# Kernel tuning notes

Measured on AMD Instinct MI355X. Metric: run time of the kernel, lower is better.

## Reference

```python
import jax, jax.numpy as jnp
import numpy as np

N = 10000   # nodes
E = 100000  # edges (before self-loops)
H = 4       # heads (layers 0-3); last layer uses 1 head
C = 200     # out_channels per head
IN_DIMS = [200, H * C, H * C, H * C, H * C]
HEADS   = [H, H, H, H, 1]
NEG_SLOPE = 0.2  # PyG GATConv default


def _gat_layer(x, src, dst, W, a_src, a_dst, b, heads):
    # x: [N, Fin], W: [Fin, heads*C], a_src/a_dst: [heads, C], b: [heads*C]
    h = (x @ W).reshape(N, heads, C)                       # [N,H,C]
    alpha_src = jnp.einsum('nhc,hc->nh', h, a_src)         # [N,H]
    alpha_dst = jnp.einsum('nhc,hc->nh', h, a_dst)         # [N,H]
    e = jax.nn.leaky_relu(alpha_src[src] + alpha_dst[dst], NEG_SLOPE)  # [E',H]
    # segment softmax over incoming edges of each dst node
    m = jax.ops.segment_max(e, dst, num_segments=N)        # [N,H]
    ex = jnp.exp(e - m[dst])                               # [E',H]
    den = jax.ops.segment_sum(ex, dst, num_segments=N)     # [N,H]
    alpha = ex / den[dst]                                  # [E',H]
    out = jax.ops.segment_sum(h[src] * alpha[:, :, None], dst, num_segments=N)
    return out.reshape(N, heads * C) + b, alpha


def setup_inputs() -> dict:
    key = jax.random.key(0)
    ks = jax.random.split(key, 2 + 4 * 5)
    inp = {}
    inp['X'] = jax.random.normal(ks[0], (N, 200), jnp.float32)
    inp['edge_index'] = jax.random.randint(ks[1], (2, E), 0, N, dtype=jnp.int32)
    k = 2
    for i in range(5):
        fin, hd = IN_DIMS[i], HEADS[i]
        s = 1.0 / np.sqrt(fin)
        inp[f'W{i}'] = jax.random.normal(ks[k], (fin, hd * C), jnp.float32) * s; k += 1
        inp[f'as{i}'] = jax.random.normal(ks[k], (hd, C), jnp.float32) * s; k += 1
        inp[f'ad{i}'] = jax.random.normal(ks[k], (hd, C), jnp.float32) * s; k += 1
        inp[f'b{i}'] = jnp.zeros((hd * C,), jnp.float32); k += 1
    return inp


def reference(X, edge_index,
              W0, as0, ad0, b0, W1, as1, ad1, b1, W2, as2, ad2, b2,
              W3, as3, ad3, b3, W4, as4, ad4, b4):
    # add self-loops (PyG GATConv default add_self_loops=True)
    loops = jnp.arange(N, dtype=edge_index.dtype)
    src = jnp.concatenate([edge_index[0], loops])
    dst = jnp.concatenate([edge_index[1], loops])
    gelu = lambda v: jax.nn.gelu(v, approximate=False)
    # eval mode: all dropouts are identity
    x, _ = _gat_layer(X, src, dst, W0, as0, ad0, b0, HEADS[0]); x = gelu(x)
    x, _ = _gat_layer(x, src, dst, W1, as1, ad1, b1, HEADS[1]); x = gelu(x)
    x, _ = _gat_layer(x, src, dst, W2, as2, ad2, b2, HEADS[2]); x = gelu(x)
    x, _ = _gat_layer(x, src, dst, W3, as3, ad3, b3, HEADS[3]); x = gelu(x)
    x, edge_attn = _gat_layer(x, src, dst, W4, as4, ad4, b4, HEADS[4])
    x = gelu(x)
    return (x, edge_attn)
```

## Files before the change

### kernel.cpp

```cpp
#include <hip/hip_runtime.h>
#include <math.h>

#define NN 10000
#define EE 100000
#define EPE 110000
#define CC 200
#define MPAD 10112

typedef __attribute__((ext_vector_type(8))) _Float16 f16x8;
typedef __attribute__((ext_vector_type(4))) _Float16 f16x4;
typedef __attribute__((ext_vector_type(4))) unsigned short u16x4;
typedef __attribute__((ext_vector_type(4))) float f32x4;

__device__ __forceinline__ float lrelu(float v) { return v >= 0.f ? v : 0.2f * v; }
__device__ __forceinline__ float gelu_f(float v) { return 0.5f * v * (1.f + erff(v * 0.70710678118654752f)); }


__global__ void build_edges_kernel(const int* __restrict__ ei,
                                   int* __restrict__ src_all, int* __restrict__ dst_all,
                                   int* __restrict__ deg) {
    int e = blockIdx.x * blockDim.x + threadIdx.x;
    if (e >= EPE) return;
    int s, d;
    if (e < EE) { s = ei[e]; d = ei[EE + e]; }
    else        { s = e - EE; d = e - EE; }
    src_all[e] = s;
    dst_all[e] = d;
    atomicAdd(&deg[d], 1);
}

__global__ void scan_kernel(const int* __restrict__ deg, int* __restrict__ row_ptr, int n) {
    __shared__ int wsum[16];
    int tid = threadIdx.x;
    int lane = tid & 63, w = tid >> 6;
    int carry = 0;
    for (int base = 0; base < n; base += 1024) {
        int idx = base + tid;
        int v = (idx < n) ? deg[idx] : 0;
        int x = v;
#pragma unroll
        for (int off = 1; off < 64; off <<= 1) {
            int t = __shfl_up(x, off);
            if (lane >= off) x += t;
        }
        if (lane == 63) wsum[w] = x;
        __syncthreads();
        if (w == 0) {
            int s = (lane < 16) ? wsum[lane] : 0;
#pragma unroll
            for (int off = 1; off < 16; off <<= 1) {
                int t = __shfl_up(s, off);
                if (lane >= off) s += t;
            }
            if (lane < 16) wsum[lane] = s;
        }
        __syncthreads();
        int woff = (w > 0) ? wsum[w - 1] : 0;
        if (idx < n) row_ptr[idx] = carry + woff + x - v;
        carry += wsum[15];
        __syncthreads();
    }
    if (tid == 0) row_ptr[n] = carry;
}

__global__ void scatter_kernel(const int* __restrict__ src_all, const int* __restrict__ dst_all,
                               const int* __restrict__ row_ptr, int* __restrict__ cursor,
                               int* __restrict__ col_src, int* __restrict__ col_eid) {
    int e = blockIdx.x * blockDim.x + threadIdx.x;
    if (e >= EPE) return;
    int d = dst_all[e];
    int pos = row_ptr[d] + atomicAdd(&cursor[d], 1);
    col_src[pos] = src_all[e];
    col_eid[pos] = e;
}


__global__ void convA_kernel(const float* __restrict__ x, int sx, int Fin, int Kp,
                             unsigned short* __restrict__ Ap) {
    size_t idx = (size_t)blockIdx.x * 256 + threadIdx.x;
    if (idx >= (size_t)MPAD * Kp) return;
    int row = (int)(idx / Kp);
    int kk  = (int)(idx % Kp);
    float v = 0.f;
    if (row < NN && kk < Fin) v = x[(size_t)row * sx + kk];
    Ap[idx] = __builtin_bit_cast(unsigned short, (_Float16)v);
}

__global__ void padA_kernel(unsigned short* __restrict__ Ap) {
    int idx = blockIdx.x * 256 + threadIdx.x;
    if (idx < NN * 32) {
        int rw = idx >> 5, c = idx & 31;
        Ap[(size_t)rw * 832 + 800 + c] = 0;
    } else {
        int j = idx - NN * 32;
        if (j < (MPAD - NN) * 832) {
            int rw = j / 832, c = j - rw * 832;
            Ap[(size_t)(NN + rw) * 832 + c] = 0;
        }
    }
}

__global__ void convB_all_kernel(const float* __restrict__ W0, const float* __restrict__ W1,
                                 const float* __restrict__ W2, const float* __restrict__ W3,
                                 const float* __restrict__ W4,
                                 unsigned short* __restrict__ Bp) {
    int l = blockIdx.y;
    const float* W = (l == 0) ? W0 : (l == 1) ? W1 : (l == 2) ? W2 : (l == 3) ? W3 : W4;
    int Fin = (l == 0) ? 200 : 800;
    int HC  = (l == 4) ? 200 : 800;
    int Kp  = (l == 0) ? 256 : 832;
    int Np  = (l == 4) ? 256 : 896;
    int idx = blockIdx.x * 256 + threadIdx.x;
    if (idx >= Np * Kp) return;
    int n = idx / Kp, kk = idx - n * Kp;
    float v = 0.f;
    if (n < HC && kk < Fin) v = W[(size_t)kk * HC + n];
    Bp[(size_t)l * (896 * 832) + idx] = __builtin_bit_cast(unsigned short, (_Float16)v);
}


__global__ __launch_bounds__(256) void gemm_mfma(const unsigned short* __restrict__ A,
                                                 const unsigned short* __restrict__ B,
                                                 unsigned short* __restrict__ C,
                                                 const float* __restrict__ a_s,
                                                 const float* __restrict__ a_d,
                                                 float* __restrict__ g_as,
                                                 float* __restrict__ g_ad,
                                                 int Kt, int Np, int ncol, int HC, int H) {
    __shared__ unsigned short As[2][4096];
    __shared__ unsigned short Bs[2][4096];

    int tid = threadIdx.x;
    int lane = tid & 63, wave = tid >> 6;

    int nwg = gridDim.x;
    int orig = blockIdx.x;
    int q = nwg >> 3, r = nwg & 7;
    int xcd = orig & 7, sidx = orig >> 3;
    int wg = (xcd < r ? xcd * (q + 1) : r * (q + 1) + (xcd - r) * q) + sidx;
    int rowT = wg / ncol, colT = wg - rowT * ncol;
    int row0 = rowT * 64, col0 = colT * 64;
    int wr = wave >> 1, wc = wave & 1;

    size_t gAoff[2], gBoff[2];
    int ldsSeg[2];
#pragma unroll
    for (int i = 0; i < 2; ++i) {
        int seg = wave * 2 + i;
        int chunkIdx = seg * 64 + lane;
        int rr = chunkIdx >> 3;
        int c = chunkIdx & 7;
        int cg = c ^ (rr & 7);
        gAoff[i] = (size_t)(row0 + rr) * Kt + (size_t)cg * 8;
        gBoff[i] = (size_t)(col0 + rr) * Kt + (size_t)cg * 8;
        ldsSeg[i] = seg * 512;
    }

    int rowA[2], rowB[2];
#pragma unroll
    for (int m = 0; m < 2; ++m) rowA[m] = wr * 32 + m * 16 + (lane & 15);
#pragma unroll
    for (int n = 0; n < 2; ++n) rowB[n] = wc * 32 + n * 16 + (lane & 15);

    int iaOff[2][2], ibOff[2][2];
#pragma unroll
    for (int kh = 0; kh < 2; ++kh) {
        int cw = kh * 4 + (lane >> 4);
#pragma unroll
        for (int m = 0; m < 2; ++m)
            iaOff[kh][m] = rowA[m] * 64 + ((cw ^ (rowA[m] & 7)) << 3);
#pragma unroll
        for (int n = 0; n < 2; ++n)
            ibOff[kh][n] = rowB[n] * 64 + ((cw ^ (rowB[n] & 7)) << 3);
    }

    f32x4 acc[2][2];
#pragma unroll
    for (int m = 0; m < 2; ++m)
#pragma unroll
        for (int n = 0; n < 2; ++n) acc[m][n] = f32x4{0.f, 0.f, 0.f, 0.f};

#define STAGE(bufi, kk)                                                                     \
    _Pragma("unroll")                                                                       \
    for (int i = 0; i < 2; ++i) {                                                           \
        __builtin_amdgcn_global_load_lds(                                                   \
            (const __attribute__((address_space(1))) void*)(A + gAoff[i] + (kk)),           \
            (__attribute__((address_space(3))) void*)(&As[bufi][ldsSeg[i]]), 16, 0, 0);     \
        __builtin_amdgcn_global_load_lds(                                                   \
            (const __attribute__((address_space(1))) void*)(B + gBoff[i] + (kk)),           \
            (__attribute__((address_space(3))) void*)(&Bs[bufi][ldsSeg[i]]), 16, 0, 0);     \
    }

    int nk = Kt >> 6;
    STAGE(0, 0)

    for (int t = 0; t < nk; ++t) {
        int cur = t & 1;
        if (t + 1 < nk) {
            STAGE(1 - cur, (t + 1) * 64)
            asm volatile("s_waitcnt vmcnt(4)" ::: "memory");
        } else {
            asm volatile("s_waitcnt vmcnt(0)" ::: "memory");
        }
        __builtin_amdgcn_s_barrier();
        __builtin_amdgcn_sched_barrier(0);

        const unsigned short* asb = As[cur];
        const unsigned short* bsb = Bs[cur];
#pragma unroll
        for (int kh = 0; kh < 2; ++kh) {
            f16x8 a[2], b[2];
#pragma unroll
            for (int m = 0; m < 2; ++m) a[m] = *(const f16x8*)(&asb[iaOff[kh][m]]);
#pragma unroll
            for (int n = 0; n < 2; ++n) b[n] = *(const f16x8*)(&bsb[ibOff[kh][n]]);
            if (kh == 0) __builtin_amdgcn_s_setprio(1);
#pragma unroll
            for (int m = 0; m < 2; ++m)
#pragma unroll
                for (int n = 0; n < 2; ++n)
                    acc[m][n] = __builtin_amdgcn_mfma_f32_16x16x32_f16(a[m], b[n], acc[m][n], 0, 0, 0);
        }
        __builtin_amdgcn_s_setprio(0);
        asm volatile("s_waitcnt lgkmcnt(0)" ::: "memory");
        __builtin_amdgcn_sched_barrier(0);
        __builtin_amdgcn_s_barrier();
        __builtin_amdgcn_sched_barrier(0);
    }
#undef STAGE

    int crow = row0 + wr * 32 + ((lane >> 4) << 2);
    int ccol = col0 + wc * 32 + (lane & 15);
#pragma unroll
    for (int m = 0; m < 2; ++m)
#pragma unroll
        for (int j = 0; j < 4; ++j) {
            size_t rb = (size_t)(crow + m * 16 + j) * Np;
#pragma unroll
            for (int n = 0; n < 2; ++n)
                C[rb + ccol + n * 16] =
                    __builtin_bit_cast(unsigned short, (_Float16)acc[m][n][j]);
        }

    int base = col0 + wc * 32;
    int hA = base / CC;
    float sAs[2][8], sAd[2][8];
#pragma unroll
    for (int b = 0; b < 2; ++b)
#pragma unroll
        for (int k = 0; k < 8; ++k) { sAs[b][k] = 0.f; sAd[b][k] = 0.f; }
#pragma unroll
    for (int n = 0; n < 2; ++n) {
        int c = ccol + n * 16;
        if (c < HC) {
            int hd = c / CC;
            int cm = c - hd * CC;
            float asv = a_s[hd * CC + cm];
            float adv = a_d[hd * CC + cm];
            int b = hd - hA;
#pragma unroll
            for (int m = 0; m < 2; ++m)
#pragma unroll
                for (int j = 0; j < 4; ++j) {
                    sAs[b][m * 4 + j] += acc[m][n][j] * asv;
                    sAd[b][m * 4 + j] += acc[m][n][j] * adv;
                }
        }
    }
#pragma unroll
    for (int off = 1; off < 16; off <<= 1) {
#pragma unroll
        for (int b = 0; b < 2; ++b)
#pragma unroll
            for (int k = 0; k < 8; ++k) {
                sAs[b][k] += __shfl_xor(sAs[b][k], off);
                sAd[b][k] += __shfl_xor(sAd[b][k], off);
            }
    }
    if ((lane & 15) == 0) {
        int slice = colT * 2 + wc;
        float* pas = g_as + (size_t)slice * NN * H;
        float* pad2 = g_ad + (size_t)slice * NN * H;
#pragma unroll
        for (int b = 0; b < 2; ++b) {
            int hd = hA + b;
            if (hd >= H) continue;
#pragma unroll
            for (int m = 0; m < 2; ++m)
#pragma unroll
                for (int j = 0; j < 4; ++j) {
                    int row = crow + m * 16 + j;
                    if (row < NN) {
                        pas[row * H + hd] = sAs[b][m * 4 + j];
                        pad2[row * H + hd] = sAd[b][m * 4 + j];
                    }
                }
        }
    }
}

__global__ void fold_attn_kernel(const float* __restrict__ g_as, const float* __restrict__ g_ad,
                                 float* __restrict__ asrc, float* __restrict__ adst, int H) {
    int i = blockIdx.x * 256 + threadIdx.x;
    if (i >= NN * H) return;
    int hd = i % H;
    int w0 = (CC * hd) >> 5, w1 = (CC * hd + CC - 1) >> 5;
    float sa = 0.f, sd = 0.f;
    for (int w = w0; w <= w1; ++w) {
        sa += g_as[(size_t)w * NN * H + i];
        sd += g_ad[(size_t)w * NN * H + i];
    }
    asrc[i] = sa;
    adst[i] = sd;
}


__global__ __launch_bounds__(256) void fused_agg_kernel(const unsigned short* __restrict__ h,
                                                        const float* __restrict__ asrc,
                                                        const float* __restrict__ adst,
                                                        const int* __restrict__ row_ptr,
                                                        const int* __restrict__ col_src,
                                                        const int* __restrict__ col_eid,
                                                        const float* __restrict__ bias,
                                                        float* __restrict__ out32,
                                                        unsigned short* __restrict__ apn,
                                                        float* __restrict__ wout,
                                                        int H, int HC, int HCp) {
    int n = blockIdx.x;
    int tid = threadIdx.x;
    int wave = tid >> 6, lane = tid & 63;
    int beg = row_ptr[n], end = row_ptr[n + 1];

    __shared__ float m_s[4], inv_s[4], ad_s[4];
    __shared__ float w_lds[64 * 4];
    __shared__ int src_lds[64];

    if (wave < H) {
        float ad = adst[n * H + wave];
        float m = -1e30f, den = 0.f;
        for (int e = beg + lane; e < end; e += 64) {
            float v = lrelu(asrc[col_src[e] * H + wave] + ad);
            if (v > m) { den = den * expf(m - v) + 1.f; m = v; }
            else den += expf(v - m);
        }
#pragma unroll
        for (int off = 1; off < 64; off <<= 1) {
            float m2 = __shfl_xor(m, off);
            float d2 = __shfl_xor(den, off);
            float M = fmaxf(m, m2);
            den = den * expf(m - M) + d2 * expf(m2 - M);
            m = M;
        }
        if (lane == 0) { m_s[wave] = m; inv_s[wave] = 1.f / den; ad_s[wave] = ad; }
    }
    __syncthreads();

    int ch0 = tid * 4;
    int head = ch0 / CC;
    float a0 = 0.f, a1 = 0.f, a2 = 0.f, a3 = 0.f;

    for (int c0 = beg; c0 < end; c0 += 64) {
        int cnt = min(64, end - c0);
        if (wave < H && lane < cnt) {
            int e = c0 + lane;
            int s = col_src[e];
            float v = lrelu(asrc[s * H + wave] + ad_s[wave]);
            float wv = expf(v - m_s[wave]) * inv_s[wave];
            w_lds[lane * 4 + wave] = wv;
            if (wave == 0) src_lds[lane] = s;
            if (wout) wout[(size_t)col_eid[e] * H + wave] = wv;
        }
        __syncthreads();
        if (ch0 < HC) {
            f16x4 hva = {}, hvb = {};
            hva = *(const f16x4*)(h + (size_t)src_lds[0] * HCp + ch0);
            if (cnt > 1) hvb = *(const f16x4*)(h + (size_t)src_lds[1] * HCp + ch0);
            for (int j = 0; j < cnt; ++j) {
                f16x4 hvc = {};
                if (j + 2 < cnt) hvc = *(const f16x4*)(h + (size_t)src_lds[j + 2] * HCp + ch0);
                float wv = w_lds[j * 4 + head];
                a0 += wv * (float)hva[0];
                a1 += wv * (float)hva[1];
                a2 += wv * (float)hva[2];
                a3 += wv * (float)hva[3];
                hva = hvb; hvb = hvc;
            }
        }
        __syncthreads();
    }

    if (ch0 < HC) {
        float4 bv = *(const float4*)(bias + ch0);
        float g0 = gelu_f(a0 + bv.x), g1 = gelu_f(a1 + bv.y);
        float g2 = gelu_f(a2 + bv.z), g3 = gelu_f(a3 + bv.w);
        if (out32) {
            *(float4*)(out32 + (size_t)n * HC + ch0) = float4{g0, g1, g2, g3};
        } else {
            *(u16x4*)(apn + (size_t)n * 832 + ch0) = u16x4{
                __builtin_bit_cast(unsigned short, (_Float16)g0),
                __builtin_bit_cast(unsigned short, (_Float16)g1),
                __builtin_bit_cast(unsigned short, (_Float16)g2),
                __builtin_bit_cast(unsigned short, (_Float16)g3)};
        }
    }
}


extern "C" void kernel_launch(void* const* d_in, const int* in_sizes, int n_in,
                              void* d_out, int out_size, void* d_ws, size_t ws_size,
                              hipStream_t stream) {
    const float* X = (const float*)d_in[0];
    const int* ei = (const int*)d_in[1];

    char* ws = (char*)d_ws;
    size_t off = 0;
    auto alloc = [&](size_t bytes) { void* p = ws + off; off += (bytes + 255) & ~(size_t)255; return p; };

    unsigned short* Ap0 = (unsigned short*)alloc((size_t)MPAD * 256 * 2);
    unsigned short* Ap  = (unsigned short*)alloc((size_t)MPAD * 832 * 2);
    unsigned short* Bp  = (unsigned short*)alloc((size_t)5 * 896 * 832 * 2);
    unsigned short* hbuf= (unsigned short*)alloc((size_t)MPAD * 896 * 2);
    float* g_as  = (float*)alloc((size_t)28 * NN * 4 * 4);
    float* g_ad  = (float*)alloc((size_t)28 * NN * 4 * 4);
    float* attn_all = (float*)alloc((size_t)5 * 2 * NN * 4 * 4);
    int* src_all  = (int*)alloc((size_t)EPE * 4);
    int* dst_all  = (int*)alloc((size_t)EPE * 4);
    int* col_src  = (int*)alloc((size_t)EPE * 4);
    int* col_eid  = (int*)alloc((size_t)EPE * 4);
    int* row_ptr  = (int*)alloc((size_t)(NN + 1) * 4);
    int* degcur   = (int*)alloc((size_t)2 * NN * 4);
    int* deg = degcur, * cursor = degcur + NN;

    hipMemsetAsync(degcur, 0, 2 * NN * sizeof(int), stream);

    int eb = (EPE + 255) / 256;
    build_edges_kernel<<<eb, 256, 0, stream>>>(ei, src_all, dst_all, deg);
    scan_kernel<<<1, 1024, 0, stream>>>(deg, row_ptr, NN);
    scatter_kernel<<<eb, 256, 0, stream>>>(src_all, dst_all, row_ptr, cursor, col_src, col_eid);

    {
        int npad = NN * 32 + (MPAD - NN) * 832;
        padA_kernel<<<(npad + 255) / 256, 256, 0, stream>>>(Ap);
    }
    {
        size_t na = (size_t)MPAD * 256;
        convA_kernel<<<(int)((na + 255) / 256), 256, 0, stream>>>(X, 200, 200, 256, Ap0);
    }
    convB_all_kernel<<<dim3((896 * 832 + 255) / 256, 5), 256, 0, stream>>>(
        (const float*)d_in[2], (const float*)d_in[6], (const float*)d_in[10],
        (const float*)d_in[14], (const float*)d_in[18], Bp);

    for (int i = 0; i < 5; ++i) {
        int H   = (i == 4) ? 1 : 4;
        int HC  = H * CC;
        int Kp  = (i == 0) ? 256 : 832;
        int Np  = (i == 4) ? 256 : 896;
        int ncol = Np / 64;
        const unsigned short* Acur = (i == 0) ? Ap0 : Ap;
        const unsigned short* Bpl = Bp + (size_t)i * (896 * 832);
        const float* as_ = (const float*)d_in[3 + 4 * i];
        const float* ad_ = (const float*)d_in[4 + 4 * i];
        const float* b_  = (const float*)d_in[5 + 4 * i];
        float* asrc_l = attn_all + (size_t)i * 2 * NN * 4;
        float* adst_l = asrc_l + NN * 4;

        gemm_mfma<<<ncol * (MPAD / 64), 256, 0, stream>>>(Acur, Bpl, hbuf, as_, ad_,
                                                          g_as, g_ad, Kp, Np, ncol, HC, H);

        fold_attn_kernel<<<(NN * H + 255) / 256, 256, 0, stream>>>(g_as, g_ad,
                                                                   asrc_l, adst_l, H);

        float* out32 = (i == 4) ? (float*)d_out : nullptr;
        unsigned short* apn = (i == 4) ? nullptr : Ap;
        float* wout = (i == 4) ? (float*)d_out + (size_t)NN * CC : nullptr;
        fused_agg_kernel<<<NN, 256, 0, stream>>>(hbuf, asrc_l, adst_l, row_ptr, col_src,
                                                 col_eid, b_, out32, apn, wout, H, HC, Np);
    }
}
```

Before: 544.2 us.

## Enlarge GEMM tiles to 128x128 and move attention logits into a separate kernel

Grows the MFMA GEMM tile from 64x64 to 128x128, with a 4x4 accumulator grid per wave, to raise data reuse per LDS load. It replaces the double-buffered pipelined K loop with a single-buffered loop guarded by __syncthreads. The fused per-head attention-logit epilogue and the fold kernel are removed, and a new per-node attn_kernel recomputes the logits from the fp16 h buffer. This costs an extra read of h and leaves fewer workgroups for the GPU's CUs. It also loses load/compute overlap, and the logits now come from fp16-rounded features.

Result: faster. 460.4 us (-15.4%).

```diff
diff --git a/kernel.cpp b/kernel.cpp
--- a/kernel.cpp
+++ b/kernel.cpp
@@ -122,13 +122,9 @@
 __global__ __launch_bounds__(256) void gemm_mfma(const unsigned short* __restrict__ A,
                                                  const unsigned short* __restrict__ B,
                                                  unsigned short* __restrict__ C,
-                                                 const float* __restrict__ a_s,
-                                                 const float* __restrict__ a_d,
-                                                 float* __restrict__ g_as,
-                                                 float* __restrict__ g_ad,
-                                                 int Kt, int Np, int ncol, int HC, int H) {
-    __shared__ unsigned short As[2][4096];
-    __shared__ unsigned short Bs[2][4096];
+                                                 int Kt, int Np, int ncol) {
+    __shared__ unsigned short As[8192];
+    __shared__ unsigned short Bs[8192];
 
     int tid = threadIdx.x;
     int lane = tid & 63, wave = tid >> 6;
@@ -139,14 +135,14 @@
     int xcd = orig & 7, sidx = orig >> 3;
     int wg = (xcd < r ? xcd * (q + 1) : r * (q + 1) + (xcd - r) * q) + sidx;
     int rowT = wg / ncol, colT = wg - rowT * ncol;
-    int row0 = rowT * 64, col0 = colT * 64;
+    int row0 = rowT * 128, col0 = colT * 128;
     int wr = wave >> 1, wc = wave & 1;
 
-    size_t gAoff[2], gBoff[2];
-    int ldsSeg[2];
-#pragma unroll
-    for (int i = 0; i < 2; ++i) {
-        int seg = wave * 2 + i;
+    size_t gAoff[4], gBoff[4];
+    int ldsSeg[4];
+#pragma unroll
+    for (int i = 0; i < 4; ++i) {
+        int seg = wave * 4 + i;
         int chunkIdx = seg * 64 + lane;
         int rr = chunkIdx >> 3;
         int c = chunkIdx & 7;
@@ -156,162 +152,101 @@
         ldsSeg[i] = seg * 512;
     }
 
-    int rowA[2], rowB[2];
-#pragma unroll
-    for (int m = 0; m < 2; ++m) rowA[m] = wr * 32 + m * 16 + (lane & 15);
-#pragma unroll
-    for (int n = 0; n < 2; ++n) rowB[n] = wc * 32 + n * 16 + (lane & 15);
-
-    int iaOff[2][2], ibOff[2][2];
+    int rowA[4], rowB[4];
+#pragma unroll
+    for (int m = 0; m < 4; ++m) {
+        rowA[m] = wr * 64 + m * 16 + (lane & 15);
+        rowB[m] = wc * 64 + m * 16 + (lane & 15);
+    }
+
+    int iaOff[2][4], ibOff[2][4];
 #pragma unroll
     for (int kh = 0; kh < 2; ++kh) {
         int cw = kh * 4 + (lane >> 4);
 #pragma unroll
-        for (int m = 0; m < 2; ++m)
+        for (int m = 0; m < 4; ++m)
             iaOff[kh][m] = rowA[m] * 64 + ((cw ^ (rowA[m] & 7)) << 3);
 #pragma unroll
-        for (int n = 0; n < 2; ++n)
+        for (int n = 0; n < 4; ++n)
             ibOff[kh][n] = rowB[n] * 64 + ((cw ^ (rowB[n] & 7)) << 3);
     }
 
-    f32x4 acc[2][2];
-#pragma unroll
-    for (int m = 0; m < 2; ++m)
-#pragma unroll
-        for (int n = 0; n < 2; ++n) acc[m][n] = f32x4{0.f, 0.f, 0.f, 0.f};
-
-#define STAGE(bufi, kk)                                                                     \
-    _Pragma("unroll")                                                                       \
-    for (int i = 0; i < 2; ++i) {                                                           \
-        __builtin_amdgcn_global_load_lds(                                                   \
-            (const __attribute__((address_space(1))) void*)(A + gAoff[i] + (kk)),           \
-            (__attribute__((address_space(3))) void*)(&As[bufi][ldsSeg[i]]), 16, 0, 0);     \
-        __builtin_amdgcn_global_load_lds(                                                   \
-            (const __attribute__((address_space(1))) void*)(B + gBoff[i] + (kk)),           \
-            (__attribute__((address_space(3))) void*)(&Bs[bufi][ldsSeg[i]]), 16, 0, 0);     \
-    }
-
-    int nk = Kt >> 6;
-    STAGE(0, 0)
-
-    for (int t = 0; t < nk; ++t) {
-        int cur = t & 1;
-        if (t + 1 < nk) {
-            STAGE(1 - cur, (t + 1) * 64)
-            asm volatile("s_waitcnt vmcnt(4)" ::: "memory");
-        } else {
-            asm volatile("s_waitcnt vmcnt(0)" ::: "memory");
-        }
-        __builtin_amdgcn_s_barrier();
-        __builtin_amdgcn_sched_barrier(0);
-
-        const unsigned short* asb = As[cur];
-        const unsigned short* bsb = Bs[cur];
+    f32x4 acc[4][4];
+#pragma unroll
+    for (int m = 0; m < 4; ++m)
+#pragma unroll
+        for (int n = 0; n < 4; ++n) acc[m][n] = f32x4{0.f, 0.f, 0.f, 0.f};
+
+    for (int k0 = 0; k0 < Kt; k0 += 64) {
+#pragma unroll
+        for (int i = 0; i < 4; ++i) {
+            __builtin_amdgcn_global_load_lds(
+                (const __attribute__((address_space(1))) void*)(A + gAoff[i] + k0),
+                (__attribute__((address_space(3))) void*)(&As[ldsSeg[i]]), 16, 0, 0);
+            __builtin_amdgcn_global_load_lds(
+                (const __attribute__((address_space(1))) void*)(B + gBoff[i] + k0),
+                (__attribute__((address_space(3))) void*)(&Bs[ldsSeg[i]]), 16, 0, 0);
+        }
+        __syncthreads();
+
 #pragma unroll
         for (int kh = 0; kh < 2; ++kh) {
-            f16x8 a[2], b[2];
-#pragma unroll
-            for (int m = 0; m < 2; ++m) a[m] = *(const f16x8*)(&asb[iaOff[kh][m]]);
-#pragma unroll
-            for (int n = 0; n < 2; ++n) b[n] = *(const f16x8*)(&bsb[ibOff[kh][n]]);
-            if (kh == 0) __builtin_amdgcn_s_setprio(1);
-#pragma unroll
-            for (int m = 0; m < 2; ++m)
-#pragma unroll
-                for (int n = 0; n < 2; ++n)
+            f16x8 a[4], b[4];
+#pragma unroll
+            for (int m = 0; m < 4; ++m) a[m] = *(const f16x8*)(&As[iaOff[kh][m]]);
+#pragma unroll
+            for (int n = 0; n < 4; ++n) b[n] = *(const f16x8*)(&Bs[ibOff[kh][n]]);
+#pragma unroll
+            for (int m = 0; m < 4; ++m)
+#pragma unroll
+                for (int n = 0; n < 4; ++n)
                     acc[m][n] = __builtin_amdgcn_mfma_f32_16x16x32_f16(a[m], b[n], acc[m][n], 0, 0, 0);
         }
-        __builtin_amdgcn_s_setprio(0);
-        asm volatile("s_waitcnt lgkmcnt(0)" ::: "memory");
-        __builtin_amdgcn_sched_barrier(0);
-        __builtin_amdgcn_s_barrier();
-        __builtin_amdgcn_sched_barrier(0);
-    }
-#undef STAGE
-
-    int crow = row0 + wr * 32 + ((lane >> 4) << 2);
-    int ccol = col0 + wc * 32 + (lane & 15);
-#pragma unroll
-    for (int m = 0; m < 2; ++m)
+        __syncthreads();
+    }
+
+    int crow = row0 + wr * 64 + ((lane >> 4) << 2);
+    int ccol = col0 + wc * 64 + (lane & 15);
+#pragma unroll
+    for (int m = 0; m < 4; ++m)
 #pragma unroll
         for (int j = 0; j < 4; ++j) {
             size_t rb = (size_t)(crow + m * 16 + j) * Np;
 #pragma unroll
-            for (int n = 0; n < 2; ++n)
+            for (int n = 0; n < 4; ++n)
                 C[rb + ccol + n * 16] =
                     __builtin_bit_cast(unsigned short, (_Float16)acc[m][n][j]);
         }
-
-    int base = col0 + wc * 32;
-    int hA = base / CC;
-    float sAs[2][8], sAd[2][8];
-#pragma unroll
-    for (int b = 0; b < 2; ++b)
-#pragma unroll
-        for (int k = 0; k < 8; ++k) { sAs[b][k] = 0.f; sAd[b][k] = 0.f; }
-#pragma unroll
-    for (int n = 0; n < 2; ++n) {
-        int c = ccol + n * 16;
-        if (c < HC) {
-            int hd = c / CC;
-            int cm = c - hd * CC;
-            float asv = a_s[hd * CC + cm];
-            float adv = a_d[hd * CC + cm];
-            int b = hd - hA;
-#pragma unroll
-            for (int m = 0; m < 2; ++m)
-#pragma unroll
-                for (int j = 0; j < 4; ++j) {
-                    sAs[b][m * 4 + j] += acc[m][n][j] * asv;
-                    sAd[b][m * 4 + j] += acc[m][n][j] * adv;
-                }
-        }
-    }
-#pragma unroll
-    for (int off = 1; off < 16; off <<= 1) {
-#pragma unroll
-        for (int b = 0; b < 2; ++b)
-#pragma unroll
-            for (int k = 0; k < 8; ++k) {
-                sAs[b][k] += __shfl_xor(sAs[b][k], off);
-                sAd[b][k] += __shfl_xor(sAd[b][k], off);
-            }
-    }
-    if ((lane & 15) == 0) {
-        int slice = colT * 2 + wc;
-        float* pas = g_as + (size_t)slice * NN * H;
-        float* pad2 = g_ad + (size_t)slice * NN * H;
-#pragma unroll
-        for (int b = 0; b < 2; ++b) {
-            int hd = hA + b;
-            if (hd >= H) continue;
-#pragma unroll
-            for (int m = 0; m < 2; ++m)
-#pragma unroll
-                for (int j = 0; j < 4; ++j) {
-                    int row = crow + m * 16 + j;
-                    if (row < NN) {
-                        pas[row * H + hd] = sAs[b][m * 4 + j];
-                        pad2[row * H + hd] = sAd[b][m * 4 + j];
-                    }
-                }
-        }
-    }
-}
-
-__global__ void fold_attn_kernel(const float* __restrict__ g_as, const float* __restrict__ g_ad,
-                                 float* __restrict__ asrc, float* __restrict__ adst, int H) {
-    int i = blockIdx.x * 256 + threadIdx.x;
-    if (i >= NN * H) return;
-    int hd = i % H;
-    int w0 = (CC * hd) >> 5, w1 = (CC * hd + CC - 1) >> 5;
-    float sa = 0.f, sd = 0.f;
-    for (int w = w0; w <= w1; ++w) {
-        sa += g_as[(size_t)w * NN * H + i];
-        sd += g_ad[(size_t)w * NN * H + i];
-    }
-    asrc[i] = sa;
-    adst[i] = sd;
+}
+
+
+__global__ void attn_kernel(const unsigned short* __restrict__ h,
+                            const float* __restrict__ a_s, const float* __restrict__ a_d,
+                            float* __restrict__ asrc, float* __restrict__ adst,
+                            int H, int HCp) {
+    int n = blockIdx.x;
+    int wave = threadIdx.x >> 6;
+    int lane = threadIdx.x & 63;
+    if (wave >= H) return;
+    float sa = 0.f, da = 0.f;
+    int c0 = lane * 4;
+    if (c0 < CC) {
+        f16x4 hv = *(const f16x4*)(h + (size_t)n * HCp + wave * CC + c0);
+        float4 av = *(const float4*)(a_s + wave * CC + c0);
+        float4 dv = *(const float4*)(a_d + wave * CC + c0);
+        float h0 = (float)hv[0], h1 = (float)hv[1], h2 = (float)hv[2], h3 = (float)hv[3];
+        sa = h0 * av.x + h1 * av.y + h2 * av.z + h3 * av.w;
+        da = h0 * dv.x + h1 * dv.y + h2 * dv.z + h3 * dv.w;
+    }
+#pragma unroll
+    for (int off = 32; off > 0; off >>= 1) {
+        sa += __shfl_down(sa, off);
+        da += __shfl_down(da, off);
+    }
+    if (lane == 0) {
+        asrc[n * H + wave] = sa;
+        adst[n * H + wave] = da;
+    }
 }
 
 
@@ -420,8 +355,6 @@
     unsigned short* Ap  = (unsigned short*)alloc((size_t)MPAD * 832 * 2);
     unsigned short* Bp  = (unsigned short*)alloc((size_t)5 * 896 * 832 * 2);
     unsigned short* hbuf= (unsigned short*)alloc((size_t)MPAD * 896 * 2);
-    float* g_as  = (float*)alloc((size_t)28 * NN * 4 * 4);
-    float* g_ad  = (float*)alloc((size_t)28 * NN * 4 * 4);
     float* attn_all = (float*)alloc((size_t)5 * 2 * NN * 4 * 4);
     int* src_all  = (int*)alloc((size_t)EPE * 4);
     int* dst_all  = (int*)alloc((size_t)EPE * 4);
@@ -455,7 +388,7 @@
         int HC  = H * CC;
         int Kp  = (i == 0) ? 256 : 832;
         int Np  = (i == 4) ? 256 : 896;
-        int ncol = Np / 64;
+        int ncol = Np / 128;
         const unsigned short* Acur = (i == 0) ? Ap0 : Ap;
         const unsigned short* Bpl = Bp + (size_t)i * (896 * 832);
         const float* as_ = (const float*)d_in[3 + 4 * i];
@@ -464,11 +397,9 @@
         float* asrc_l = attn_all + (size_t)i * 2 * NN * 4;
         float* adst_l = asrc_l + NN * 4;
 
-        gemm_mfma<<<ncol * (MPAD / 64), 256, 0, stream>>>(Acur, Bpl, hbuf, as_, ad_,
-                                                          g_as, g_ad, Kp, Np, ncol, HC, H);
-
-        fold_attn_kernel<<<(NN * H + 255) / 256, 256, 0, stream>>>(g_as, g_ad,
-                                                                   asrc_l, adst_l, H);
+        gemm_mfma<<<ncol * (MPAD / 128), 256, 0, stream>>>(Acur, Bpl, hbuf, Kp, Np, ncol);
+
+        attn_kernel<<<NN, 256, 0, stream>>>(hbuf, as_, ad_, asrc_l, adst_l, H, Np);
 
         float* out32 = (i == 4) ? (float*)d_out : nullptr;
         unsigned short* apn = (i == 4) ? nullptr : Ap;
```
